# Optimization experiments

Hardware: AMD Instinct MI355X
Metric: run time of the kernel (lower is better)

Reference implementation:

```python
import jax, jax.numpy as jnp
import numpy as np

# Static config (matches init_kwargs / chosen geometry)
DIM, HEADS, WS, SHIFT = 96, 3, 7, 3
H, W = 56, 56
B = 64
N = WS * WS
HID = int(DIM * 4.0)
EPS = 1e-5


def _rel_tables():
    # relative_coords_table: (1, 2*WS-1, 2*WS-1, 2), log-spaced coords in [-1,1]
    c = np.arange(-(WS - 1), WS, dtype=np.float32)
    tab = np.stack(np.meshgrid(c, c, indexing='ij'), axis=-1)[None]
    tab = tab / (WS - 1) * 8.0
    tab = np.sign(tab) * np.log2(np.abs(tab) + 1.0) / np.log2(8.0)
    # relative_position_index: (N, N) int
    coords = np.stack(np.meshgrid(np.arange(WS), np.arange(WS), indexing='ij'))
    cf = coords.reshape(2, -1)
    rel = (cf[:, :, None] - cf[:, None, :]).transpose(1, 2, 0).astype(np.int64)
    rel[..., 0] += WS - 1
    rel[..., 1] += WS - 1
    rel[..., 0] *= 2 * WS - 1
    return jnp.asarray(tab), jnp.asarray(rel.sum(-1))

_TABLE, _RPI = _rel_tables()


def _shift_mask():
    # standard SW-MSA mask: (num_windows, N, N), 0 / -100
    img = np.zeros((1, H, W, 1), dtype=np.float32)
    cnt = 0
    segs = (slice(0, -WS), slice(-WS, -SHIFT), slice(-SHIFT, None))
    for hs in segs:
        for ws_ in segs:
            img[:, hs, ws_, :] = cnt
            cnt += 1
    mw = img.reshape(1, H // WS, WS, W // WS, WS, 1).transpose(0, 1, 3, 2, 4, 5).reshape(-1, N)
    am = mw[:, None, :] - mw[:, :, None]
    return jnp.asarray(np.where(am != 0, -100.0, 0.0).astype(np.float32))


def _ln(x, g, b):
    mu = x.mean(-1, keepdims=True)
    var = x.var(-1, keepdims=True)
    return (x - mu) * jax.lax.rsqrt(var + EPS) * g + b


def setup_inputs() -> dict:
    key = jax.random.key(0)
    ks = jax.random.split(key, 8)
    s = 0.02
    return {
        'x': jax.random.normal(ks[0], (B, H * W, DIM), jnp.float32),
        'attn_mask': _shift_mask(),
        'qkv_w': jax.random.normal(ks[1], (3 * DIM, DIM), jnp.float32) * s,
        'q_bias': jnp.zeros((DIM,), jnp.float32),
        'v_bias': jnp.zeros((DIM,), jnp.float32),
        'logit_scale': jnp.full((HEADS, 1, 1), np.log(10.0), jnp.float32),
        'cpb_w1': jax.random.normal(ks[2], (512, 2), jnp.float32) * s,
        'cpb_b1': jnp.zeros((512,), jnp.float32),
        'cpb_w2': jax.random.normal(ks[3], (HEADS, 512), jnp.float32) * s,
        'proj_w': jax.random.normal(ks[4], (DIM, DIM), jnp.float32) * s,
        'proj_b': jnp.zeros((DIM,), jnp.float32),
        'norm1_g': jnp.ones((DIM,), jnp.float32),
        'norm1_b': jnp.zeros((DIM,), jnp.float32),
        'fc1_w': jax.random.normal(ks[5], (HID, DIM), jnp.float32) * s,
        'fc1_b': jnp.zeros((HID,), jnp.float32),
        'fc2_w': jax.random.normal(ks[6], (DIM, HID), jnp.float32) * s,
        'fc2_b': jnp.zeros((DIM,), jnp.float32),
        'norm2_g': jnp.ones((DIM,), jnp.float32),
        'norm2_b': jnp.zeros((DIM,), jnp.float32),
    }


def reference(x, attn_mask, qkv_w, q_bias, v_bias, logit_scale, cpb_w1, cpb_b1,
              cpb_w2, proj_w, proj_b, norm1_g, norm1_b, fc1_w, fc1_b, fc2_w,
              fc2_b, norm2_g, norm2_b):
    Bx, L, C = x.shape
    d = C // HEADS
    nH, nWd = H // WS, W // WS
    shortcut = x

    xi = x.reshape(Bx, H, W, C)
    xi = jnp.roll(xi, (-SHIFT, -SHIFT), axis=(1, 2))
    # window partition -> (Bx*nH*nWd, N, C)
    xw = xi.reshape(Bx, nH, WS, nWd, WS, C).transpose(0, 1, 3, 2, 4, 5).reshape(-1, N, C)

    # qkv with q/v bias only (k bias fixed to zero)
    qkv_bias = jnp.concatenate([q_bias, jnp.zeros_like(v_bias), v_bias])
    qkv = (xw @ qkv_w.T + qkv_bias).reshape(-1, N, 3, HEADS, d).transpose(2, 0, 3, 1, 4)
    q, k, v = qkv[0], qkv[1], qkv[2]  # (B_, h, N, d)

    # cosine attention with clamped learnable temperature
    qn = q / jnp.maximum(jnp.linalg.norm(q, axis=-1, keepdims=True), 1e-12)
    kn = k / jnp.maximum(jnp.linalg.norm(k, axis=-1, keepdims=True), 1e-12)
    attn = jnp.einsum('bhnd,bhmd->bhnm', qn, kn)
    scale = jnp.exp(jnp.minimum(logit_scale, jnp.log(jnp.float32(100.0))))
    attn = attn * scale

    # continuous relative position bias via cpb_mlp
    tab = jax.nn.gelu(_TABLE @ cpb_w1.T + cpb_b1, approximate=False) @ cpb_w2.T
    tab = tab.reshape(-1, HEADS)
    rpb = tab[_RPI.reshape(-1)].reshape(N, N, HEADS).transpose(2, 0, 1)
    attn = attn + (16.0 * jax.nn.sigmoid(rpb))[None]

    # shift mask
    nWin = attn_mask.shape[0]
    attn = attn.reshape(-1, nWin, HEADS, N, N) + attn_mask[None, :, None]
    attn = jax.nn.softmax(attn.reshape(-1, HEADS, N, N), axis=-1)

    out = jnp.einsum('bhnm,bhmd->bnhd', attn, v).reshape(-1, N, C)
    out = out @ proj_w.T + proj_b

    # window reverse + un-shift
    out = out.reshape(Bx, nH, nWd, WS, WS, C).transpose(0, 1, 3, 2, 4, 5).reshape(Bx, H, W, C)
    out = jnp.roll(out, (SHIFT, SHIFT), axis=(1, 2)).reshape(Bx, L, C)

    # SwinV2 post-norm residuals
    x1 = shortcut + _ln(out, norm1_g, norm1_b)
    h = jax.nn.gelu(x1 @ fc1_w.T + fc1_b, approximate=False) @ fc2_w.T + fc2_b
    return x1 + _ln(h, norm2_g, norm2_b)
```

## Files before the change

### kernel.cpp

```cpp
#include <hip/hip_runtime.h>
#include <math.h>

#define BATCH 64
#define HW 56
#define CDIM 96
#define NHEADS 3
#define WSZ 7
#define NTOK 49
#define SHIFT_ 3
#define NWIN_TOT 4096
#define HID 384
#define NTOKENS (BATCH * HW * HW)
#define LN100 4.6051702f

typedef __attribute__((ext_vector_type(8))) short bf16x8;
typedef __attribute__((ext_vector_type(4))) float f32x4;

__device__ inline f32x4 mfma16(bf16x8 a, bf16x8 b, f32x4 c) {
  return __builtin_amdgcn_mfma_f32_16x16x32_bf16(a, b, c, 0, 0, 0);
}

__device__ inline unsigned short f2b(float f) {
  unsigned u = __float_as_uint(f);
  unsigned r = (u + 0x7FFFu + ((u >> 16) & 1u)) >> 16;
  return (unsigned short)r;
}
__device__ inline float blo(unsigned u) { return __uint_as_float(u << 16); }
__device__ inline unsigned packb(float a, float b) {
  return (unsigned)f2b(a) | ((unsigned)f2b(b) << 16);
}
__device__ inline void split8(const float* p, bf16x8& hi, bf16x8& lo) {
  short h8[8], l8[8];
  #pragma unroll
  for (int j = 0; j < 8; ++j) {
    unsigned short h = f2b(p[j]);
    float hf = __uint_as_float((unsigned)h << 16);
    h8[j] = (short)h;
    l8[j] = (short)f2b(p[j] - hf);
  }
  hi = bf16x8{h8[0], h8[1], h8[2], h8[3], h8[4], h8[5], h8[6], h8[7]};
  lo = bf16x8{l8[0], l8[1], l8[2], l8[3], l8[4], l8[5], l8[6], l8[7]};
}
__device__ inline float gelu_f(float v) {
  float a = fabsf(v) * 0.70710678118654752f;
  float t = 1.0f / fmaf(a, 0.3275911f, 1.0f);
  float p = t * fmaf(t, fmaf(t, fmaf(t, fmaf(t, 1.061405429f, -1.453152027f),
                                     1.421413741f), -0.284496736f), 0.254829592f);
  float er = 1.0f - p * __expf(-a * a);
  er = (v < 0.f) ? -er : er;
  return 0.5f * v * (1.0f + er);
}

__global__ __launch_bounds__(256) void wconv2_kernel(
    const float* __restrict__ qkv_w, const float* __restrict__ fc1_w,
    const float* __restrict__ fc2_w, const float* __restrict__ proj_w,
    unsigned* __restrict__ qkvf, unsigned* __restrict__ w1f,
    unsigned* __restrict__ w2f, unsigned* __restrict__ pwf) {
  int T = blockIdx.x * 256 + threadIdx.x;
  if (T < 3456) {
    int tk = T >> 6, l = T & 63;
    int n = tk / 3, ks = tk - n * 3;
    int o = n * 16 + (l & 15);
    const float* src = qkv_w + o * 96 + ks * 32 + (l >> 4) * 8;
    uint4 d;
    d.x = packb(src[0], src[1]); d.y = packb(src[2], src[3]);
    d.z = packb(src[4], src[5]); d.w = packb(src[6], src[7]);
    *(uint4*)&qkvf[(size_t)(tk * 64 + l) * 4] = d;
    return;
  }
  T -= 3456;
  if (T < 4608) {
    int tk = T >> 6, l = T & 63;
    int n = tk / 3, ks = tk - n * 3;
    int o = n * 16 + (l & 15);
    const float* src = fc1_w + o * 96 + ks * 32 + (l >> 4) * 8;
    uint4 d;
    d.x = packb(src[0], src[1]); d.y = packb(src[2], src[3]);
    d.z = packb(src[4], src[5]); d.w = packb(src[6], src[7]);
    *(uint4*)&w1f[(size_t)(tk * 64 + l) * 4] = d;
    return;
  }
  T -= 4608;
  if (T < 4608) {
    int tk = T >> 6, l = T & 63;
    int n = tk / 12, ks = tk - n * 12;
    int o = n * 16 + (l & 15);
    const float* src = fc2_w + o * 384 + ks * 32 + (l >> 4) * 8;
    uint4 d;
    d.x = packb(src[0], src[1]); d.y = packb(src[2], src[3]);
    d.z = packb(src[4], src[5]); d.w = packb(src[6], src[7]);
    *(uint4*)&w2f[(size_t)(tk * 64 + l) * 4] = d;
    return;
  }
  T -= 4608;
  if (T < 1152) {
    int tk = T >> 6, l = T & 63;
    int n = tk / 3, ks = tk - n * 3;
    int o = n * 16 + (l & 15);
    const float* src = proj_w + o * 96 + ks * 32 + (l >> 4) * 8;
    uint4 d;
    d.x = packb(src[0], src[1]); d.y = packb(src[2], src[3]);
    d.z = packb(src[4], src[5]); d.w = packb(src[6], src[7]);
    *(uint4*)&pwf[(size_t)(tk * 64 + l) * 4] = d;
  }
}

__global__ __launch_bounds__(512) void cpb_table_kernel(
    const float* __restrict__ w1, const float* __restrict__ b1,
    const float* __restrict__ w2, float* __restrict__ tabout) {
  int tid = threadIdx.x;
  if (tid >= 169 * 3) return;
  int e = tid / 3, h = tid - e * 3;
  int i = e / 13, j = e - i * 13;
  float ti = (float)(i - 6) * (8.0f / 6.0f);
  float tj = (float)(j - 6) * (8.0f / 6.0f);
  float sx = (ti > 0.f) ? 1.f : (ti < 0.f ? -1.f : 0.f);
  float sy = (tj > 0.f) ? 1.f : (tj < 0.f ? -1.f : 0.f);
  float tx = sx * log2f(fabsf(ti) + 1.f) * (1.0f / 3.0f);
  float ty = sy * log2f(fabsf(tj) + 1.f) * (1.0f / 3.0f);
  float acc = 0.f;
  for (int jj = 0; jj < 512; ++jj) {
    float hv = tx * w1[jj * 2 + 0] + ty * w1[jj * 2 + 1] + b1[jj];
    float g = 0.5f * hv * (1.f + erff(hv * 0.70710678118654752f));
    acc += g * w2[h * 512 + jj];
  }
  tabout[e * 3 + h] = acc;
}

__global__ __launch_bounds__(256) void bias_kernel(
    const float* __restrict__ tabout, float* __restrict__ bias16) {
  int idx = blockIdx.x * 256 + threadIdx.x;
  if (idx >= NHEADS * NTOK * NTOK) return;
  int h = idx / (NTOK * NTOK);
  int rem = idx - h * NTOK * NTOK;
  int i = rem / NTOK, j = rem - i * NTOK;
  int ri = (i / WSZ) - (j / WSZ) + 6;
  int ci = (i % WSZ) - (j % WSZ) + 6;
  int e = ri * 13 + ci;
  float v = tabout[e * 3 + h];
  bias16[idx] = 16.f / (1.f + expf(-v));
}

__global__ __launch_bounds__(256) void qkv_mfma_kernel(
    const float* __restrict__ x, const unsigned* __restrict__ qkvf,
    const float* __restrict__ q_bias, const float* __restrict__ v_bias,
    const float* __restrict__ logit_scale,
    unsigned* __restrict__ qws, unsigned* __restrict__ kws,
    unsigned* __restrict__ vws) {
  __shared__ unsigned xa[64 * 52];
  int tid = threadIdx.x, lane = tid & 63, wv = tid >> 6;
  size_t tok0 = (size_t)blockIdx.x * 64;

  for (int idx = tid; idx < 3072; idx += 256) {
    int t = idx / 48, c2 = idx - t * 48;
    const float2 s = *(const float2*)(x + (tok0 + t) * 96 + c2 * 2);
    xa[t * 52 + c2] = packb(s.x, s.y);
  }
  __syncthreads();

  int c15 = lane & 15, q4 = lane >> 4;
  bf16x8 afr[3];
  #pragma unroll
  for (int k = 0; k < 3; ++k)
    afr[k] = *(const bf16x8*)&xa[(wv * 16 + c15) * 52 + k * 16 + q4 * 4];

  f32x4 acc[18];
  #pragma unroll
  for (int n = 0; n < 18; ++n) acc[n] = f32x4{0.f, 0.f, 0.f, 0.f};
  #pragma unroll
  for (int n = 0; n < 18; ++n) {
    #pragma unroll
    for (int k = 0; k < 3; ++k) {
      bf16x8 b = *(const bf16x8*)&qkvf[(size_t)((n * 3 + k) * 64 + lane) * 4];
      acc[n] = mfma16(afr[k], b, acc[n]);
    }
  }

  int tokr0 = (int)tok0 + wv * 16 + q4 * 4;
  #pragma unroll
  for (int h = 0; h < 3; ++h) {
    float sc = expf(fminf(logit_scale[h], LN100));
    {
      f32x4 a0 = acc[2 * h], a1 = acc[2 * h + 1];
      float b0 = q_bias[h * 32 + c15], b1 = q_bias[h * 32 + 16 + c15];
      unsigned pk[8];
      #pragma unroll
      for (int i = 0; i < 4; ++i) {
        float va = a0[i] + b0, vb = a1[i] + b1;
        float ss = va * va + vb * vb;
        ss += __shfl_xor(ss, 1, 64); ss += __shfl_xor(ss, 2, 64);
        ss += __shfl_xor(ss, 4, 64); ss += __shfl_xor(ss, 8, 64);
        float inv = sc / fmaxf(sqrtf(ss), 1e-12f);
        va *= inv; vb *= inv;
        float pa = __shfl_xor(va, 1, 64), pb = __shfl_xor(vb, 1, 64);
        pk[i] = packb(va, pa); pk[4 + i] = packb(vb, pb);
      }
      if (!(lane & 1)) {
        int dw0 = c15 >> 1;
        #pragma unroll
        for (int i = 0; i < 4; ++i) {
          size_t base = ((size_t)(tokr0 + i) * 3 + h) * 16;
          qws[base + dw0] = pk[i];
          qws[base + 8 + dw0] = pk[4 + i];
        }
      }
    }
    {
      f32x4 a0 = acc[6 + 2 * h], a1 = acc[7 + 2 * h];
      unsigned pk[8];
      #pragma unroll
      for (int i = 0; i < 4; ++i) {
        float va = a0[i], vb = a1[i];
        float ss = va * va + vb * vb;
        ss += __shfl_xor(ss, 1, 64); ss += __shfl_xor(ss, 2, 64);
        ss += __shfl_xor(ss, 4, 64); ss += __shfl_xor(ss, 8, 64);
        float inv = 1.f / fmaxf(sqrtf(ss), 1e-12f);
        va *= inv; vb *= inv;
        float pa = __shfl_xor(va, 1, 64), pb = __shfl_xor(vb, 1, 64);
        pk[i] = packb(va, pa); pk[4 + i] = packb(vb, pb);
      }
      if (!(lane & 1)) {
        int dw0 = c15 >> 1;
        #pragma unroll
        for (int i = 0; i < 4; ++i) {
          size_t base = ((size_t)(tokr0 + i) * 3 + h) * 16;
          kws[base + dw0] = pk[i];
          kws[base + 8 + dw0] = pk[4 + i];
        }
      }
    }
    {
      f32x4 a0 = acc[12 + 2 * h], a1 = acc[13 + 2 * h];
      float b0 = v_bias[h * 32 + c15], b1 = v_bias[h * 32 + 16 + c15];
      unsigned pk[8];
      #pragma unroll
      for (int i = 0; i < 4; ++i) {
        float va = a0[i] + b0, vb = a1[i] + b1;
        float pa = __shfl_xor(va, 1, 64), pb = __shfl_xor(vb, 1, 64);
        pk[i] = packb(va, pa); pk[4 + i] = packb(vb, pb);
      }
      if (!(lane & 1)) {
        int dw0 = c15 >> 1;
        #pragma unroll
        for (int i = 0; i < 4; ++i) {
          size_t base = ((size_t)(tokr0 + i) * 3 + h) * 16;
          vws[base + dw0] = pk[i];
          vws[base + 8 + dw0] = pk[4 + i];
        }
      }
    }
  }
}

__global__ __launch_bounds__(256) void attn_fused_kernel(
    const unsigned* __restrict__ qws, const unsigned* __restrict__ kws,
    const unsigned* __restrict__ vws, const float* __restrict__ bias16,
    const float* __restrict__ mask, const unsigned* __restrict__ pwf,
    const float* __restrict__ proj_b, const float* __restrict__ x,
    const float* __restrict__ n1g, const float* __restrict__ n1b,
    float* __restrict__ out) {
  __shared__ int toks[64];
  __shared__ unsigned short VtS[3 * 32 * 72];
  __shared__ float Pf[3 * 64 * 68];
  __shared__ unsigned obuf[64 * 52];

  int tid = threadIdx.x, lane = tid & 63, wv = tid >> 6;
  int c15 = lane & 15, q4 = lane >> 4;
  int win = blockIdx.x;
  int b = win >> 6, wi = win & 63, wh = wi >> 3, wcx = wi & 7;

  if (tid < 64) {
    int t = tid < 49 ? tid : 48;
    int tr = (t * 9363) >> 16, tc = t - tr * 7;
    int R = wh * 7 + tr + SHIFT_; if (R >= HW) R -= HW;
    int C = wcx * 7 + tc + SHIFT_; if (C >= HW) C -= HW;
    toks[tid] = b * 3136 + R * 56 + C;
  }
  __syncthreads();

  bf16x8 qf[4], kf[4];
  if (wv < 3) {
    #pragma unroll
    for (int m = 0; m < 4; ++m)
      qf[m] = *(const bf16x8*)&qws[((size_t)toks[m * 16 + c15] * 3 + wv) * 16 + q4 * 4];
    #pragma unroll
    for (int n = 0; n < 4; ++n)
      kf[n] = *(const bf16x8*)&kws[((size_t)toks[n * 16 + c15] * 3 + wv) * 16 + q4 * 4];
  }

  for (int idx = tid; idx < 768; idx += 256) {
    int h2 = idx >> 8, rem = idx & 255;
    int t = rem >> 2, dg = rem & 3;
    uint4 v4 = *(const uint4*)&vws[((size_t)toks[t] * 3 + h2) * 16 + dg * 4];
    unsigned short* dst = &VtS[h2 * 2304 + (dg * 8) * 72 + t];
    dst[0 * 72] = (unsigned short)(v4.x & 0xFFFFu); dst[1 * 72] = (unsigned short)(v4.x >> 16);
    dst[2 * 72] = (unsigned short)(v4.y & 0xFFFFu); dst[3 * 72] = (unsigned short)(v4.y >> 16);
    dst[4 * 72] = (unsigned short)(v4.z & 0xFFFFu); dst[5 * 72] = (unsigned short)(v4.z >> 16);
    dst[6 * 72] = (unsigned short)(v4.w & 0xFFFFu); dst[7 * 72] = (unsigned short)(v4.w >> 16);
  }
  __syncthreads();

  if (wv < 3) {
    int h = wv;
    f32x4 s[4][4];
    #pragma unroll
    for (int m = 0; m < 4; ++m)
      #pragma unroll
      for (int n = 0; n < 4; ++n)
        s[m][n] = mfma16(qf[m], kf[n], f32x4{0.f, 0.f, 0.f, 0.f});

    const float* bsl = bias16 + h * 2401;
    const float* msl = mask + (size_t)wi * 2401;
    #pragma unroll
    for (int m = 0; m < 4; ++m) {
      #pragma unroll
      for (int i = 0; i < 4; ++i) {
        int rw = m * 16 + 4 * q4 + i;
        if (rw < 49) {
          const float* br = bsl + rw * 49;
          const float* mr = msl + rw * 49;
          #pragma unroll
          for (int n = 0; n < 4; ++n) {
            int j = n * 16 + c15;
            s[m][n][i] = (j < 49) ? (s[m][n][i] + br[j] + mr[j]) : -1e30f;
          }
        } else {
          #pragma unroll
          for (int n = 0; n < 4; ++n)
            if (n * 16 + c15 >= 49) s[m][n][i] = -1e30f;
        }
      }
    }

    #pragma unroll
    for (int m = 0; m < 4; ++m) {
      #pragma unroll
      for (int i = 0; i < 4; ++i) {
        float mx = fmaxf(fmaxf(s[m][0][i], s[m][1][i]), fmaxf(s[m][2][i], s[m][3][i]));
        mx = fmaxf(mx, __shfl_xor(mx, 1, 64)); mx = fmaxf(mx, __shfl_xor(mx, 2, 64));
        mx = fmaxf(mx, __shfl_xor(mx, 4, 64)); mx = fmaxf(mx, __shfl_xor(mx, 8, 64));
        float sum = 0.f;
        #pragma unroll
        for (int n = 0; n < 4; ++n) { float e = __expf(s[m][n][i] - mx); s[m][n][i] = e; sum += e; }
        sum += __shfl_xor(sum, 1, 64); sum += __shfl_xor(sum, 2, 64);
        sum += __shfl_xor(sum, 4, 64); sum += __shfl_xor(sum, 8, 64);
        float inv = 1.f / sum;
        #pragma unroll
        for (int n = 0; n < 4; ++n) s[m][n][i] *= inv;
      }
    }

    #pragma unroll
    for (int m = 0; m < 4; ++m)
      #pragma unroll
      for (int n = 0; n < 4; ++n)
        #pragma unroll
        for (int i = 0; i < 4; ++i)
          Pf[h * 4352 + (m * 16 + 4 * q4 + i) * 68 + n * 16 + c15] = s[m][n][i];
    asm volatile("s_waitcnt lgkmcnt(0)" ::: "memory");
    __builtin_amdgcn_sched_barrier(0);

    f32x4 o[4][2];
    #pragma unroll
    for (int m = 0; m < 4; ++m)
      #pragma unroll
      for (int n2 = 0; n2 < 2; ++n2) o[m][n2] = f32x4{0.f, 0.f, 0.f, 0.f};
    #pragma unroll
    for (int ks = 0; ks < 2; ++ks) {
      bf16x8 phi[4], plo[4];
      #pragma unroll
      for (int m = 0; m < 4; ++m) {
        float p8[8];
        const float* src = &Pf[h * 4352 + (m * 16 + c15) * 68 + ks * 32 + q4 * 8];
        *(float4*)&p8[0] = *(const float4*)&src[0];
        *(float4*)&p8[4] = *(const float4*)&src[4];
        split8(p8, phi[m], plo[m]);
      }
      #pragma unroll
      for (int n2 = 0; n2 < 2; ++n2) {
        bf16x8 vb = *(const bf16x8*)&VtS[h * 2304 + (n2 * 16 + c15) * 72 + ks * 32 + q4 * 8];
        #pragma unroll
        for (int m = 0; m < 4; ++m) {
          o[m][n2] = mfma16(phi[m], vb, o[m][n2]);
          o[m][n2] = mfma16(plo[m], vb, o[m][n2]);
        }
      }
    }

    #pragma unroll
    for (int m = 0; m < 4; ++m)
      #pragma unroll
      for (int n2 = 0; n2 < 2; ++n2)
        #pragma unroll
        for (int i = 0; i < 4; ++i) {
          float ov = o[m][n2][i];
          float on = __shfl_xor(ov, 1, 64);
          if (!(lane & 1))
            obuf[(m * 16 + 4 * q4 + i) * 52 + h * 16 + n2 * 8 + (c15 >> 1)] = packb(ov, on);
        }
  }
  __syncthreads();

  bf16x8 oa[3];
  #pragma unroll
  for (int ks = 0; ks < 3; ++ks)
    oa[ks] = *(const bf16x8*)&obuf[(wv * 16 + c15) * 52 + ks * 16 + q4 * 4];
  f32x4 pr[6];
  #pragma unroll
  for (int n = 0; n < 6; ++n) pr[n] = f32x4{0.f, 0.f, 0.f, 0.f};
  #pragma unroll
  for (int n = 0; n < 6; ++n)
    #pragma unroll
    for (int ks = 0; ks < 3; ++ks) {
      bf16x8 bfr = *(const bf16x8*)&pwf[(size_t)((n * 3 + ks) * 64 + lane) * 4];
      pr[n] = mfma16(oa[ks], bfr, pr[n]);
    }

  float* ybuf = (float*)Pf;
  #pragma unroll
  for (int n = 0; n < 6; ++n) {
    int col = n * 16 + c15;
    float bo = proj_b[col];
    #pragma unroll
    for (int i = 0; i < 4; ++i)
      ybuf[(wv * 16 + 4 * q4 + i) * 100 + col] = pr[n][i] + bo;
  }
  __syncthreads();

  int t = tid >> 2, pp = tid & 3;
  if (t < 49) {
    const float* yrow = ybuf + t * 100 + pp * 24;
    float s1 = 0.f;
    #pragma unroll
    for (int c = 0; c < 24; ++c) s1 += yrow[c];
    s1 += __shfl_xor(s1, 1, 64); s1 += __shfl_xor(s1, 2, 64);
    float mu = s1 * (1.f / 96.f);
    float v2 = 0.f;
    #pragma unroll
    for (int c = 0; c < 24; ++c) { float d = yrow[c] - mu; v2 += d * d; }
    v2 += __shfl_xor(v2, 1, 64); v2 += __shfl_xor(v2, 2, 64);
    float rs = rsqrtf(v2 * (1.f / 96.f) + 1e-5f);
    size_t base = (size_t)toks[t] * 96 + pp * 24;
    #pragma unroll
    for (int c4 = 0; c4 < 6; ++c4) {
      float4 xv = *(const float4*)(x + base + c4 * 4);
      float4 gv = *(const float4*)(n1g + pp * 24 + c4 * 4);
      float4 bv = *(const float4*)(n1b + pp * 24 + c4 * 4);
      float4 ov;
      ov.x = xv.x + (yrow[c4 * 4 + 0] - mu) * rs * gv.x + bv.x;
      ov.y = xv.y + (yrow[c4 * 4 + 1] - mu) * rs * gv.y + bv.y;
      ov.z = xv.z + (yrow[c4 * 4 + 2] - mu) * rs * gv.z + bv.z;
      ov.w = xv.w + (yrow[c4 * 4 + 3] - mu) * rs * gv.w + bv.w;
      *(float4*)(out + base + c4 * 4) = ov;
    }
  }
}

__global__ __launch_bounds__(256) void mlp_mfma_kernel(
    const unsigned* __restrict__ w1f, const float* __restrict__ fc1_b,
    const unsigned* __restrict__ w2f, const float* __restrict__ fc2_b,
    const float* __restrict__ n2g, const float* __restrict__ n2b,
    float* __restrict__ xio) {
  __shared__ unsigned xa[64 * 52];
  __shared__ unsigned hid[64 * 196];
  __shared__ float mu_s[64], rs_s[64];
  int tid = threadIdx.x, lane = tid & 63, wv = tid >> 6;
  int c15 = lane & 15, q4 = lane >> 4;
  size_t tok0 = (size_t)blockIdx.x * 64;

  for (int idx = tid; idx < 3072; idx += 256) {
    int t = idx / 48, c2 = idx - t * 48;
    const float2 s = *(const float2*)(xio + (tok0 + t) * 96 + c2 * 2);
    xa[t * 52 + c2] = packb(s.x, s.y);
  }
  __syncthreads();

  bf16x8 afr[4][3];
  #pragma unroll
  for (int m = 0; m < 4; ++m)
    #pragma unroll
    for (int k = 0; k < 3; ++k)
      afr[m][k] = *(const bf16x8*)&xa[(m * 16 + c15) * 52 + k * 16 + q4 * 4];
  f32x4 acc[4][6];
  #pragma unroll
  for (int m = 0; m < 4; ++m)
    #pragma unroll
    for (int n = 0; n < 6; ++n) acc[m][n] = f32x4{0.f, 0.f, 0.f, 0.f};
  #pragma unroll
  for (int n = 0; n < 6; ++n) {
    #pragma unroll
    for (int k = 0; k < 3; ++k) {
      bf16x8 b = *(const bf16x8*)&w1f[(size_t)(((6 * wv + n) * 3 + k) * 64 + lane) * 4];
      #pragma unroll
      for (int m = 0; m < 4; ++m) acc[m][n] = mfma16(afr[m][k], b, acc[m][n]);
    }
  }
  unsigned short* hidb = (unsigned short*)hid;
  #pragma unroll
  for (int n = 0; n < 6; ++n) {
    int col = (6 * wv + n) * 16 + c15;
    float bo = fc1_b[col];
    #pragma unroll
    for (int m = 0; m < 4; ++m) {
      #pragma unroll
      for (int i = 0; i < 4; ++i) {
        float g = gelu_f(acc[m][n][i] + bo);
        hidb[(m * 16 + q4 * 4 + i) * 392 + col] = f2b(g);
      }
    }
  }
  __syncthreads();

  f32x4 acc2[6];
  #pragma unroll
  for (int n = 0; n < 6; ++n) acc2[n] = f32x4{0.f, 0.f, 0.f, 0.f};
  #pragma unroll
  for (int k = 0; k < 12; ++k) {
    bf16x8 a = *(const bf16x8*)&hid[(wv * 16 + c15) * 196 + k * 16 + q4 * 4];
    #pragma unroll
    for (int n = 0; n < 6; ++n) {
      bf16x8 b = *(const bf16x8*)&w2f[(size_t)((n * 12 + k) * 64 + lane) * 4];
      acc2[n] = mfma16(a, b, acc2[n]);
    }
  }
  __syncthreads();

  float* ybuf = (float*)hid;
  #pragma unroll
  for (int n = 0; n < 6; ++n) {
    int col = n * 16 + c15;
    float bo = fc2_b[col];
    #pragma unroll
    for (int i = 0; i < 4; ++i)
      ybuf[(wv * 16 + q4 * 4 + i) * 100 + col] = acc2[n][i] + bo;
  }
  __syncthreads();

  {
    int t = tid >> 2, p = tid & 3;
    const float* row = ybuf + t * 100 + p * 24;
    float s = 0.f, s2 = 0.f;
    for (int c = 0; c < 24; ++c) { float v = row[c]; s += v; s2 += v * v; }
    s += __shfl_xor(s, 1, 64); s2 += __shfl_xor(s2, 1, 64);
    s += __shfl_xor(s, 2, 64); s2 += __shfl_xor(s2, 2, 64);
    if (p == 0) {
      float mu = s * (1.f / 96.f);
      float var = s2 * (1.f / 96.f) - mu * mu;
      mu_s[t] = mu;
      rs_s[t] = rsqrtf(fmaxf(var, 0.f) + 1e-5f);
    }
  }
  __syncthreads();

  for (int idx = tid; idx < 6144; idx += 256) {
    int t = idx / 96, c = idx - t * 96;
    float y = ybuf[t * 100 + c];
    xio[tok0 * 96 + idx] += (y - mu_s[t]) * rs_s[t] * n2g[c] + n2b[c];
  }
}

extern "C" void kernel_launch(void* const* d_in, const int* in_sizes, int n_in,
                              void* d_out, int out_size, void* d_ws, size_t ws_size,
                              hipStream_t stream) {
  const float* x           = (const float*)d_in[0];
  const float* attn_mask   = (const float*)d_in[1];
  const float* qkv_w       = (const float*)d_in[2];
  const float* q_bias      = (const float*)d_in[3];
  const float* v_bias      = (const float*)d_in[4];
  const float* logit_scale = (const float*)d_in[5];
  const float* cpb_w1      = (const float*)d_in[6];
  const float* cpb_b1      = (const float*)d_in[7];
  const float* cpb_w2      = (const float*)d_in[8];
  const float* proj_w      = (const float*)d_in[9];
  const float* proj_b      = (const float*)d_in[10];
  const float* n1g         = (const float*)d_in[11];
  const float* n1b         = (const float*)d_in[12];
  const float* fc1_w       = (const float*)d_in[13];
  const float* fc1_b       = (const float*)d_in[14];
  const float* fc2_w       = (const float*)d_in[15];
  const float* fc2_b       = (const float*)d_in[16];
  const float* n2g         = (const float*)d_in[17];
  const float* n2b         = (const float*)d_in[18];
  float* out = (float*)d_out;

  float* tab     = (float*)d_ws;
  float* bias16  = tab + 512;
  unsigned* qkvf = (unsigned*)(bias16 + 7296);
  unsigned* w1f  = qkvf + 13824;
  unsigned* w2f  = w1f + 18432;
  unsigned* pwf  = w2f + 18432;
  unsigned* qws  = pwf + 4608;
  unsigned* kws  = qws + 9633792;
  unsigned* vws  = kws + 9633792;

  wconv2_kernel<<<54, 256, 0, stream>>>(qkv_w, fc1_w, fc2_w, proj_w,
                                        qkvf, w1f, w2f, pwf);
  cpb_table_kernel<<<1, 512, 0, stream>>>(cpb_w1, cpb_b1, cpb_w2, tab);
  bias_kernel<<<(NHEADS * NTOK * NTOK + 255) / 256, 256, 0, stream>>>(tab, bias16);
  qkv_mfma_kernel<<<NTOKENS / 64, 256, 0, stream>>>(x, qkvf, q_bias, v_bias,
                                                    logit_scale, qws, kws, vws);
  attn_fused_kernel<<<NWIN_TOT, 256, 0, stream>>>(qws, kws, vws, bias16, attn_mask,
                                                  pwf, proj_b, x, n1g, n1b, out);
  mlp_mfma_kernel<<<NTOKENS / 64, 256, 0, stream>>>(w1f, fc1_b, w2f, fc2_b,
                                                    n2g, n2b, out);
}
```

Measured before the change: 495.9 us.

## Use fp16 P and V in attention PV matmul and shrink shared memory

Replaces the split bf16 hi/lo emulation of fp32 P in the PV product with a single fp16 MFMA, storing P as fp16 in an XOR-swizzled shared buffer and converting V to fp16. This halves the PV MFMA count and removes the split conversion work and fp32 P storage. It also aliases shared buffers in both the attention and MLP kernels to cut LDS use, which may allow more blocks per CU. The cost is one extra barrier in the MLP kernel and a precision change: P now carries fp16 rounding instead of near-fp32 accuracy.

```diff
diff --git a/kernel.cpp b/kernel.cpp
--- a/kernel.cpp
+++ b/kernel.cpp
@@ -14,10 +14,14 @@
 #define LN100 4.6051702f
 
 typedef __attribute__((ext_vector_type(8))) short bf16x8;
+typedef __attribute__((ext_vector_type(8))) _Float16 f16x8;
 typedef __attribute__((ext_vector_type(4))) float f32x4;
 
 __device__ inline f32x4 mfma16(bf16x8 a, bf16x8 b, f32x4 c) {
   return __builtin_amdgcn_mfma_f32_16x16x32_bf16(a, b, c, 0, 0, 0);
+}
+__device__ inline f32x4 mfma16h(f16x8 a, f16x8 b, f32x4 c) {
+  return __builtin_amdgcn_mfma_f32_16x16x32_f16(a, b, c, 0, 0, 0);
 }
 
 __device__ inline unsigned short f2b(float f) {
@@ -26,20 +30,9 @@
   return (unsigned short)r;
 }
 __device__ inline float blo(unsigned u) { return __uint_as_float(u << 16); }
+__device__ inline float bhi(unsigned u) { return __uint_as_float(u & 0xFFFF0000u); }
 __device__ inline unsigned packb(float a, float b) {
   return (unsigned)f2b(a) | ((unsigned)f2b(b) << 16);
-}
-__device__ inline void split8(const float* p, bf16x8& hi, bf16x8& lo) {
-  short h8[8], l8[8];
-  #pragma unroll
-  for (int j = 0; j < 8; ++j) {
-    unsigned short h = f2b(p[j]);
-    float hf = __uint_as_float((unsigned)h << 16);
-    h8[j] = (short)h;
-    l8[j] = (short)f2b(p[j] - hf);
-  }
-  hi = bf16x8{h8[0], h8[1], h8[2], h8[3], h8[4], h8[5], h8[6], h8[7]};
-  lo = bf16x8{l8[0], l8[1], l8[2], l8[3], l8[4], l8[5], l8[6], l8[7]};
 }
 __device__ inline float gelu_f(float v) {
   float a = fabsf(v) * 0.70710678118654752f;
@@ -259,10 +252,12 @@
     const float* __restrict__ proj_b, const float* __restrict__ x,
     const float* __restrict__ n1g, const float* __restrict__ n1b,
     float* __restrict__ out) {
-  __shared__ int toks[64];
-  __shared__ unsigned short VtS[3 * 32 * 72];
-  __shared__ float Pf[3 * 64 * 68];
-  __shared__ unsigned obuf[64 * 52];
+  __shared__ __align__(16) unsigned smem[12992];
+  _Float16* VtS  = (_Float16*)smem;
+  _Float16* Ph   = (_Float16*)((char*)smem + 13824);
+  unsigned* obuf = (unsigned*)((char*)smem + 38400);
+  int*      toks = (int*)((char*)smem + 51712);
+  float*    ybuf = (float*)smem;
 
   int tid = threadIdx.x, lane = tid & 63, wv = tid >> 6;
   int c15 = lane & 15, q4 = lane >> 4;
@@ -292,11 +287,11 @@
     int h2 = idx >> 8, rem = idx & 255;
     int t = rem >> 2, dg = rem & 3;
     uint4 v4 = *(const uint4*)&vws[((size_t)toks[t] * 3 + h2) * 16 + dg * 4];
-    unsigned short* dst = &VtS[h2 * 2304 + (dg * 8) * 72 + t];
-    dst[0 * 72] = (unsigned short)(v4.x & 0xFFFFu); dst[1 * 72] = (unsigned short)(v4.x >> 16);
-    dst[2 * 72] = (unsigned short)(v4.y & 0xFFFFu); dst[3 * 72] = (unsigned short)(v4.y >> 16);
-    dst[4 * 72] = (unsigned short)(v4.z & 0xFFFFu); dst[5 * 72] = (unsigned short)(v4.z >> 16);
-    dst[6 * 72] = (unsigned short)(v4.w & 0xFFFFu); dst[7 * 72] = (unsigned short)(v4.w >> 16);
+    _Float16* dst = &VtS[h2 * 2304 + (dg * 8) * 72 + t];
+    dst[0 * 72] = (_Float16)blo(v4.x); dst[1 * 72] = (_Float16)bhi(v4.x);
+    dst[2 * 72] = (_Float16)blo(v4.y); dst[3 * 72] = (_Float16)bhi(v4.y);
+    dst[4 * 72] = (_Float16)blo(v4.z); dst[5 * 72] = (_Float16)bhi(v4.z);
+    dst[6 * 72] = (_Float16)blo(v4.w); dst[7 * 72] = (_Float16)bhi(v4.w);
   }
   __syncthreads();
 
@@ -353,10 +348,15 @@
     #pragma unroll
     for (int m = 0; m < 4; ++m)
       #pragma unroll
-      for (int n = 0; n < 4; ++n)
-        #pragma unroll
-        for (int i = 0; i < 4; ++i)
-          Pf[h * 4352 + (m * 16 + 4 * q4 + i) * 68 + n * 16 + c15] = s[m][n][i];
+      for (int n = 0; n < 4; ++n) {
+        int gw = n * 2 + (c15 >> 3);
+        #pragma unroll
+        for (int i = 0; i < 4; ++i) {
+          int row = m * 16 + 4 * q4 + i;
+          int gp = gw ^ (row & 7);
+          Ph[h * 4096 + row * 64 + gp * 8 + (c15 & 7)] = (_Float16)s[m][n][i];
+        }
+      }
     asm volatile("s_waitcnt lgkmcnt(0)" ::: "memory");
     __builtin_amdgcn_sched_barrier(0);
 
@@ -367,23 +367,18 @@
       for (int n2 = 0; n2 < 2; ++n2) o[m][n2] = f32x4{0.f, 0.f, 0.f, 0.f};
     #pragma unroll
     for (int ks = 0; ks < 2; ++ks) {
-      bf16x8 phi[4], plo[4];
+      f16x8 pa[4];
       #pragma unroll
       for (int m = 0; m < 4; ++m) {
-        float p8[8];
-        const float* src = &Pf[h * 4352 + (m * 16 + c15) * 68 + ks * 32 + q4 * 8];
-        *(float4*)&p8[0] = *(const float4*)&src[0];
-        *(float4*)&p8[4] = *(const float4*)&src[4];
-        split8(p8, phi[m], plo[m]);
+        int row = m * 16 + c15;
+        int gp = (ks * 4 + q4) ^ (c15 & 7);
+        pa[m] = *(const f16x8*)&Ph[h * 4096 + row * 64 + gp * 8];
       }
       #pragma unroll
       for (int n2 = 0; n2 < 2; ++n2) {
-        bf16x8 vb = *(const bf16x8*)&VtS[h * 2304 + (n2 * 16 + c15) * 72 + ks * 32 + q4 * 8];
-        #pragma unroll
-        for (int m = 0; m < 4; ++m) {
-          o[m][n2] = mfma16(phi[m], vb, o[m][n2]);
-          o[m][n2] = mfma16(plo[m], vb, o[m][n2]);
-        }
+        f16x8 vb = *(const f16x8*)&VtS[h * 2304 + (n2 * 16 + c15) * 72 + ks * 32 + q4 * 8];
+        #pragma unroll
+        for (int m = 0; m < 4; ++m) o[m][n2] = mfma16h(pa[m], vb, o[m][n2]);
       }
     }
 
@@ -416,7 +411,6 @@
       pr[n] = mfma16(oa[ks], bfr, pr[n]);
     }
 
-  float* ybuf = (float*)Pf;
   #pragma unroll
   for (int n = 0; n < 6; ++n) {
     int col = n * 16 + c15;
@@ -461,9 +455,11 @@
     const unsigned* __restrict__ w2f, const float* __restrict__ fc2_b,
     const float* __restrict__ n2g, const float* __restrict__ n2b,
     float* __restrict__ xio) {
-  __shared__ unsigned xa[64 * 52];
-  __shared__ unsigned hid[64 * 196];
+  __shared__ __align__(16) unsigned mlpbuf[12544];
   __shared__ float mu_s[64], rs_s[64];
+  unsigned* xa  = mlpbuf;
+  unsigned* hid = mlpbuf;
+  float*   ybuf = (float*)mlpbuf;
   int tid = threadIdx.x, lane = tid & 63, wv = tid >> 6;
   int c15 = lane & 15, q4 = lane >> 4;
   size_t tok0 = (size_t)blockIdx.x * 64;
@@ -481,6 +477,8 @@
     #pragma unroll
     for (int k = 0; k < 3; ++k)
       afr[m][k] = *(const bf16x8*)&xa[(m * 16 + c15) * 52 + k * 16 + q4 * 4];
+  __syncthreads();
+
   f32x4 acc[4][6];
   #pragma unroll
   for (int m = 0; m < 4; ++m)
@@ -525,7 +523,6 @@
   }
   __syncthreads();
 
-  float* ybuf = (float*)hid;
   #pragma unroll
   for (int n = 0; n < 6; ++n) {
     int col = n * 16 + c15;
```

New measurement: 546.6 us. 1.1x slower.
